# Optimization experiments

Measured on AMD Instinct MI355X. Metric: run time of the kernel, lower is better.

Reference implementation:

```python
import jax, jax.numpy as jnp
import numpy as np

B, T = 512, 200
N_SKILLS, M, DK, DV, H = 1000, 50, 64, 64, 128


def setup_inputs() -> dict:
    key = jax.random.key(0)
    ks = jax.random.split(key, 12)
    inp = {
        'skill_seq': jax.random.randint(ks[0], (B, T), 0, N_SKILLS, dtype=jnp.int32),
        'correct_seq': jax.random.randint(ks[1], (B, T), 0, 2, dtype=jnp.int32),
        'mask': jnp.ones((B, T), dtype=jnp.float32),
        'skill_embed': jax.random.normal(ks[2], (N_SKILLS, DK), dtype=jnp.float32),
        'key_memory': jax.random.normal(ks[3], (M, DK), dtype=jnp.float32) * 0.1,
        'value_init': jnp.zeros((M, DV), dtype=jnp.float32),
        'interaction_embed': jax.random.normal(ks[4], (2 * N_SKILLS, DV), dtype=jnp.float32),
        'erase_W': jax.random.normal(ks[5], (DV, DV), dtype=jnp.float32) * 0.05,
        'erase_b': jnp.zeros((DV,), dtype=jnp.float32),
        'add_W': jax.random.normal(ks[6], (DV, DV), dtype=jnp.float32) * 0.05,
        'add_b': jnp.zeros((DV,), dtype=jnp.float32),
        'fc1_W': jax.random.normal(ks[7], (DK + DV, H), dtype=jnp.float32) * 0.05,
        'fc1_b': jnp.zeros((H,), dtype=jnp.float32),
        'fc2_W': jax.random.normal(ks[8], (H, 1), dtype=jnp.float32) * 0.05,
        'fc2_b': jnp.zeros((1,), dtype=jnp.float32),
    }
    return inp


def reference(skill_seq, correct_seq, mask, skill_embed, key_memory, value_init,
              interaction_embed, erase_W, erase_b, add_W, add_b,
              fc1_W, fc1_b, fc2_W, fc2_b):
    n_skills = skill_embed.shape[0]
    b = skill_seq.shape[0]
    # Time-invariant-per-step quantities are precomputed vectorized over (B,T):
    q = skill_embed[skill_seq]                                   # (B,T,dk)
    w = jax.nn.softmax(jnp.einsum('btk,mk->btm', q, key_memory), axis=-1)  # (B,T,M)
    v = interaction_embed[skill_seq + correct_seq * n_skills]    # (B,T,dv)
    e = jax.nn.sigmoid(v @ erase_W + erase_b)                    # (B,T,dv)
    a = jnp.tanh(v @ add_W + add_b)                              # (B,T,dv)

    def step(mem, inputs):
        # mem: (B,M,dv); read BEFORE write, matching the torch loop
        w_t, e_t, a_t = inputs                                   # (B,M),(B,dv),(B,dv)
        read = jnp.einsum('bm,bmv->bv', w_t, mem)                # (B,dv)
        we = w_t[:, :, None]                                     # (B,M,1)
        mem = mem * (1.0 - we * e_t[:, None, :]) + we * a_t[:, None, :]
        return mem, read

    mem0 = jnp.broadcast_to(value_init, (b,) + value_init.shape)
    _, reads = jax.lax.scan(step, mem0,
                            (jnp.swapaxes(w, 0, 1), jnp.swapaxes(e, 0, 1), jnp.swapaxes(a, 0, 1)))
    reads = jnp.swapaxes(reads, 0, 1)                            # (B,T,dv)

    x = jnp.concatenate([q, reads], axis=-1)                     # (B,T,dk+dv)
    h = jax.nn.relu(x @ fc1_W + fc1_b)
    logit = (h @ fc2_W + fc2_b)[..., 0]
    p = jax.nn.sigmoid(logit)
    return p * mask, correct_seq.astype(jnp.float32) * mask
```

## Files before the change

### kernel.cpp

```cpp
#include <hip/hip_runtime.h>
#include <hip/hip_bf16.h>

#define B_  512
#define T_  200
#define NS  1000
#define M_  50
#define DK  64
#define DV  64
#define H_  128
#define NPOS (B_ * T_)

typedef __hip_bfloat16 bf16;
typedef unsigned short ushort_t;
typedef __bf16 bf16x8 __attribute__((ext_vector_type(8)));
typedef float  f32x4  __attribute__((ext_vector_type(4)));

__device__ __forceinline__ float ldf(const void* p, int i, int isbf) {
    return isbf ? __bfloat162float(((const bf16*)p)[i]) : ((const float*)p)[i];
}
__device__ __forceinline__ int sniff(const void* mask) {
    return (*(const unsigned*)mask == 0x3F800000u) ? 0 : 1;
}
__device__ __forceinline__ float rl(float x, int l) {
    return __int_as_float(__builtin_amdgcn_readlane(__float_as_int(x), l));
}
__device__ __forceinline__ ushort_t f2bf(float v) {
    bf16 h = __float2bfloat16(v);
    return *(ushort_t*)&h;
}

__global__ __launch_bounds__(256) void dk25_tabs(
    const void* __restrict__ mask,
    const void* __restrict__ skill_embed, const void* __restrict__ key_memory,
    const void* __restrict__ inter,
    const void* __restrict__ eW, const void* __restrict__ eb,
    const void* __restrict__ aW, const void* __restrict__ ab,
    const void* __restrict__ fc1W, const void* __restrict__ fc1b,
    float* __restrict__ w_tab, unsigned* __restrict__ ea_tab,
    float* __restrict__ hq_tab, ushort_t* __restrict__ W2f) {
    int isbf = sniff(mask);
    int lane = threadIdx.x & 63;
    int gwid = (blockIdx.x << 2) | (threadIdx.x >> 6);

    if (gwid < NS) {
        int s = gwid;
        float q = ldf(skill_embed, s * DK + lane, isbf);
        float acc = 0.f;
        if (lane < M_) {
            #pragma unroll 16
            for (int k = 0; k < DK; ++k)
                acc = fmaf(rl(q, k), ldf(key_memory, lane * DK + k, isbf), acc);
        }
        float val = (lane < M_) ? acc : -1e30f;
        float mx = val;
        #pragma unroll
        for (int off = 1; off < 64; off <<= 1) mx = fmaxf(mx, __shfl_xor(mx, off, 64));
        float ex = (lane < M_) ? __expf(val - mx) : 0.f;
        float sm = ex;
        #pragma unroll
        for (int off = 1; off < 64; off <<= 1) sm += __shfl_xor(sm, off, 64);
        w_tab[s * 64 + lane] = (lane < M_) ? ex / sm : 0.f;
    } else if (gwid < 3 * NS) {
        int r = gwid - NS;
        float vv = ldf(inter, r * DV + lane, isbf);
        float eacc = ldf(eb, lane, isbf);
        float aacc = ldf(ab, lane, isbf);
        #pragma unroll 16
        for (int u = 0; u < DV; ++u) {
            float vu = rl(vv, u);
            eacc = fmaf(vu, ldf(eW, u * DV + lane, isbf), eacc);
            aacc = fmaf(vu, ldf(aW, u * DV + lane, isbf), aacc);
        }
        float ev = 1.f / (1.f + __expf(-eacc));
        float av = tanhf(aacc);
        ea_tab[r * 64 + lane] = ((unsigned)f2bf(av) << 16) | (unsigned)f2bf(ev);
    } else if (gwid < 4 * NS) {
        int s = gwid - 3 * NS;
        float q = ldf(skill_embed, s * DK + lane, isbf);
        float acc0 = ldf(fc1b, lane, isbf);
        float acc1 = ldf(fc1b, 64 + lane, isbf);
        #pragma unroll 16
        for (int k = 0; k < DK; ++k) {
            float qk = rl(q, k);
            acc0 = fmaf(qk, ldf(fc1W, k * H_ + lane, isbf), acc0);
            acc1 = fmaf(qk, ldf(fc1W, k * H_ + 64 + lane, isbf), acc1);
        }
        hq_tab[s * H_ + lane]      = acc0;
        hq_tab[s * H_ + 64 + lane] = acc1;
    } else if (gwid < 4 * NS + 16) {
        int f = gwid - 4 * NS;
        int tile = f >> 1, kk = f & 1;
        int n = tile * 16 + (lane & 15);
        #pragma unroll
        for (int j = 0; j < 8; ++j) {
            int v = kk * 32 + (lane >> 4) * 8 + j;
            W2f[(f * 64 + lane) * 8 + j] = f2bf(ldf(fc1W, (DK + v) * H_ + n, isbf));
        }
    }
}


#define WAITV(N) \
    asm volatile("s_waitcnt vmcnt(" #N ")" ::: "memory"); \
    __builtin_amdgcn_sched_barrier(0);

#define GLL(gsrc, ldst) \
    __builtin_amdgcn_global_load_lds( \
        (const __attribute__((address_space(1))) void*)(const void*)(gsrc), \
        (__attribute__((address_space(3))) void*)(void*)(ldst), 4, 0, 0);

#define ISSUE(NB) { \
    _Pragma("unroll") \
    for (int st = 0; st < 8; ++st) { \
        const float*    wsrc_  = w_tab  + sI[st] * 64 + lane; \
        const unsigned* easrc_ = ea_tab + (sI[st] + cI[st] * NS) * 64 + lane; \
        GLL(wsrc_,  &ldsw[NB][st][0]) \
        GLL(easrc_, &ldsea[NB][st][0]) \
    } }

#define SCROW(W, MEM) \
    acc0 = fmaf(W.x, MEM.x, acc0); \
    acc1 = fmaf(W.y, MEM.y, acc1); \
    acc2 = fmaf(W.z, MEM.z, acc2); \
    acc3 = fmaf(W.w, MEM.w, acc3); \
    MEM.x = fmaf(-W.x, fmaf(e0, MEM.x, -a0), MEM.x); \
    MEM.y = fmaf(-W.y, fmaf(e0, MEM.y, -a0), MEM.y); \
    MEM.z = fmaf(-W.z, fmaf(e0, MEM.z, -a0), MEM.z); \
    MEM.w = fmaf(-W.w, fmaf(e0, MEM.w, -a0), MEM.w);

#define PSTEP(NB, TP) { \
    unsigned ea = ldsea[NB][TP][lane]; \
    float e0 = __uint_as_float(ea << 16); \
    float a0 = __uint_as_float(ea & 0xFFFF0000u); \
    float acc0 = 0.f, acc1 = 0.f, acc2 = 0.f, acc3 = 0.f; \
    { float4 w = ldsw[NB][TP][4 * k + 0]; SCROW(w, mem[0]) } \
    { float4 w = ldsw[NB][TP][4 * k + 1]; SCROW(w, mem[1]) } \
    { float4 w = ldsw[NB][TP][4 * k + 2]; SCROW(w, mem[2]) } \
    { float4 w = ldsw[NB][TP][4 * k + 3]; SCROW(w, mem[3]) } \
    read_bf[outbase + (TP) * 256] = f2bf((acc0 + acc1) + (acc2 + acc3)); }

__global__ __launch_bounds__(64, 2) void dk25_scan(
    const int*  __restrict__ ss, const int* __restrict__ cs,
    const void* __restrict__ mask, const void* __restrict__ value_init,
    const float* __restrict__ w_tab, const unsigned* __restrict__ ea_tab,
    ushort_t* __restrict__ read_bf) {

    __shared__ float4   ldsw[2][8][16];
    __shared__ unsigned ldsea[2][8][64];

    int isbf = sniff(mask);
    int lane = threadIdx.x;
    int bk   = blockIdx.x;
    int b    = bk >> 2, k = bk & 3;
    const int base = b * T_;

    float4 mem[4];
    #pragma unroll
    for (int i = 0; i < 4; ++i) {
        int r = 16 * k + 4 * i;
        mem[i].x = (r + 0 < M_) ? ldf(value_init, (r + 0) * DV + lane, isbf) : 0.f;
        mem[i].y = (r + 1 < M_) ? ldf(value_init, (r + 1) * DV + lane, isbf) : 0.f;
        mem[i].z = (r + 2 < M_) ? ldf(value_init, (r + 2) * DV + lane, isbf) : 0.f;
        mem[i].w = (r + 3 < M_) ? ldf(value_init, (r + 3) * DV + lane, isbf) : 0.f;
    }

    int sI[8], cI[8];

    #pragma unroll
    for (int st = 0; st < 8; ++st) { sI[st] = ss[base + st];     cI[st] = cs[base + st]; }
    ISSUE(0)
    #pragma unroll
    for (int st = 0; st < 8; ++st) { sI[st] = ss[base + 8 + st]; cI[st] = cs[base + 8 + st]; }
    ISSUE(1)

    size_t outbase = ((size_t)base * 4 + k) * 64 + lane;

    for (int cc = 0; cc < 25; ++cc) {
        int nb = cc & 1;
        int tb2 = 8 * (cc + 2); if (tb2 > T_ - 8) tb2 = T_ - 8;
        #pragma unroll
        for (int st = 0; st < 8; ++st) {
            sI[st] = ss[base + tb2 + st]; cI[st] = cs[base + tb2 + st];
        }
        WAITV(16)
        PSTEP(nb, 0) PSTEP(nb, 1) PSTEP(nb, 2) PSTEP(nb, 3)
        PSTEP(nb, 4) PSTEP(nb, 5) PSTEP(nb, 6) PSTEP(nb, 7)
        __builtin_amdgcn_sched_barrier(0);
        ISSUE(nb)
        __builtin_amdgcn_sched_barrier(0);
        outbase += 2048;
    }
}

#define FOR8(X) X(0) X(1) X(2) X(3) X(4) X(5) X(6) X(7)
#define DECL_C(t)  f32x4 c##t = {0.f, 0.f, 0.f, 0.f};
#define LOADB(t) bf16x8 b##t##_0 = B8[(2 * (t)) * 64 + lane], \
                        b##t##_1 = B8[(2 * (t) + 1) * 64 + lane];
#define FCKK(kk, p) { \
    bf16x8 av = A8[col * 32 + (kk) * 4 + quad]; \
    c0 = __builtin_amdgcn_mfma_f32_16x16x32_bf16(av, b0_##p, c0, 0, 0, 0); \
    c1 = __builtin_amdgcn_mfma_f32_16x16x32_bf16(av, b1_##p, c1, 0, 0, 0); \
    c2 = __builtin_amdgcn_mfma_f32_16x16x32_bf16(av, b2_##p, c2, 0, 0, 0); \
    c3 = __builtin_amdgcn_mfma_f32_16x16x32_bf16(av, b3_##p, c3, 0, 0, 0); \
    c4 = __builtin_amdgcn_mfma_f32_16x16x32_bf16(av, b4_##p, c4, 0, 0, 0); \
    c5 = __builtin_amdgcn_mfma_f32_16x16x32_bf16(av, b5_##p, c5, 0, 0, 0); \
    c6 = __builtin_amdgcn_mfma_f32_16x16x32_bf16(av, b6_##p, c6, 0, 0, 0); \
    c7 = __builtin_amdgcn_mfma_f32_16x16x32_bf16(av, b7_##p, c7, 0, 0, 0); }
#define EPI(t) { \
    float h; \
    h = c##t.x + hq_tab[s0r * H_ + t * 16 + col]; x0 = fmaf(fmaxf(h, 0.f), f2w##t, x0); \
    h = c##t.y + hq_tab[s1r * H_ + t * 16 + col]; x1 = fmaf(fmaxf(h, 0.f), f2w##t, x1); \
    h = c##t.z + hq_tab[s2r * H_ + t * 16 + col]; x2 = fmaf(fmaxf(h, 0.f), f2w##t, x2); \
    h = c##t.w + hq_tab[s3r * H_ + t * 16 + col]; x3 = fmaf(fmaxf(h, 0.f), f2w##t, x3); }

__global__ __launch_bounds__(64)
__attribute__((amdgpu_waves_per_eu(3))) void dk25_fc(
    const int*  __restrict__ skill_seq, const int* __restrict__ correct_seq,
    const void* __restrict__ mask,
    const void* __restrict__ fc2W, const void* __restrict__ fc2b,
    const float* __restrict__ hq_tab, const ushort_t* __restrict__ W2f,
    const ushort_t* __restrict__ read_bf,
    float* __restrict__ out0, float* __restrict__ out1) {

    int isbf = sniff(mask);
    int lane = threadIdx.x;
    int col  = lane & 15, quad = lane >> 4;

    const bf16x8* B8 = (const bf16x8*)W2f;
    FOR8(LOADB)

    float f2w0 = ldf(fc2W,   0 + col, isbf), f2w1 = ldf(fc2W,  16 + col, isbf);
    float f2w2 = ldf(fc2W,  32 + col, isbf), f2w3 = ldf(fc2W,  48 + col, isbf);
    float f2w4 = ldf(fc2W,  64 + col, isbf), f2w5 = ldf(fc2W,  80 + col, isbf);
    float f2w6 = ldf(fc2W,  96 + col, isbf), f2w7 = ldf(fc2W, 112 + col, isbf);
    float f2b  = ldf(fc2b, 0, isbf);

    for (int pg = blockIdx.x; pg < NPOS / 16; pg += gridDim.x) {
        int p0 = pg * 16;
        const bf16x8* A8 = (const bf16x8*)(read_bf + (size_t)p0 * 256);

        int s0r = skill_seq[p0 + quad * 4 + 0];
        int s1r = skill_seq[p0 + quad * 4 + 1];
        int s2r = skill_seq[p0 + quad * 4 + 2];
        int s3r = skill_seq[p0 + quad * 4 + 3];

        FOR8(DECL_C)
        FCKK(0, 0) FCKK(1, 1) FCKK(2, 0) FCKK(3, 1)
        FCKK(4, 0) FCKK(5, 1) FCKK(6, 0) FCKK(7, 1)

        float x0 = 0.f, x1 = 0.f, x2 = 0.f, x3 = 0.f;
        FOR8(EPI)

        #pragma unroll
        for (int off = 1; off < 16; off <<= 1) {
            x0 += __shfl_xor(x0, off, 64);
            x1 += __shfl_xor(x1, off, 64);
            x2 += __shfl_xor(x2, off, 64);
            x3 += __shfl_xor(x3, off, 64);
        }

        float mk0 = ldf(mask, p0 + quad * 4 + 0, isbf);
        float mk1 = ldf(mask, p0 + quad * 4 + 1, isbf);
        float mk2 = ldf(mask, p0 + quad * 4 + 2, isbf);
        float mk3 = ldf(mask, p0 + quad * 4 + 3, isbf);
        if (col == 0) {
            out0[p0 + quad * 4 + 0] = mk0 / (1.f + __expf(-(x0 + f2b)));
            out0[p0 + quad * 4 + 1] = mk1 / (1.f + __expf(-(x1 + f2b)));
            out0[p0 + quad * 4 + 2] = mk2 / (1.f + __expf(-(x2 + f2b)));
            out0[p0 + quad * 4 + 3] = mk3 / (1.f + __expf(-(x3 + f2b)));
        }
        if (col == 1) {
            out1[p0 + quad * 4 + 0] = (float)correct_seq[p0 + quad * 4 + 0] * mk0;
            out1[p0 + quad * 4 + 1] = (float)correct_seq[p0 + quad * 4 + 1] * mk1;
            out1[p0 + quad * 4 + 2] = (float)correct_seq[p0 + quad * 4 + 2] * mk2;
            out1[p0 + quad * 4 + 3] = (float)correct_seq[p0 + quad * 4 + 3] * mk3;
        }
    }
}

extern "C" void kernel_launch(void* const* d_in, const int* in_sizes, int n_in,
                              void* d_out, int out_size, void* d_ws, size_t ws_size,
                              hipStream_t stream) {
    const int*  skill_seq   = (const int*)d_in[0];
    const int*  correct_seq = (const int*)d_in[1];
    const void* mask        = d_in[2];
    const void* skill_embed = d_in[3];
    const void* key_memory  = d_in[4];
    const void* value_init  = d_in[5];
    const void* inter       = d_in[6];
    const void* erase_W     = d_in[7];
    const void* erase_b     = d_in[8];
    const void* add_W       = d_in[9];
    const void* add_b       = d_in[10];
    const void* fc1_W       = d_in[11];
    const void* fc1_b       = d_in[12];
    const void* fc2_W       = d_in[13];
    const void* fc2_b       = d_in[14];
    float* out = (float*)d_out;

    float*    ws      = (float*)d_ws + 16;
    float*    w_tab   = ws;
    unsigned* ea_tab  = (unsigned*)(ws + 64000);
    float*    hq_tab  = ws + 192000;
    ushort_t* W2f     = (ushort_t*)(ws + 320000);
    ushort_t* read_bf = (ushort_t*)(ws + 336400);

    dk25_tabs<<<1004, 256, 0, stream>>>(mask, skill_embed, key_memory, inter,
                                        erase_W, erase_b, add_W, add_b,
                                        fc1_W, fc1_b,
                                        w_tab, ea_tab, hq_tab, W2f);

    dk25_scan<<<B_ * 4, 64, 0, stream>>>(skill_seq, correct_seq, mask, value_init,
                                         w_tab, ea_tab, read_bf);

    dk25_fc<<<3200, 64, 0, stream>>>(skill_seq, correct_seq, mask,
                                     fc2_W, fc2_b, hq_tab, W2f, read_bf,
                                     out, out + (size_t)NPOS);
}
```

Before: 196.0 us.

## Replace LDS-staged scan prefetch with register double-buffered loads; permute hq table

The scan kernel no longer stages w and erase/add rows through LDS with global_load_lds and manual vmcnt waits. It keeps two register sets (A/B) and refills one directly from global memory right after each step consumes it, prefetching indices a chunk ahead. The hq table is also stored in a permuted layout so the FC epilogue fetches each row's hq values with two vector loads instead of eight scalar gathers. The scan change removes LDS traffic and waits but leaves only one step of latency hiding, so load stalls may surface.

```diff
diff --git a/kernel.cpp b/kernel.cpp
--- a/kernel.cpp
+++ b/kernel.cpp
@@ -29,7 +29,7 @@
     return *(ushort_t*)&h;
 }
 
-__global__ __launch_bounds__(256) void dk25_tabs(
+__global__ __launch_bounds__(256) void dk27_tabs(
     const void* __restrict__ mask,
     const void* __restrict__ skill_embed, const void* __restrict__ key_memory,
     const void* __restrict__ inter,
@@ -37,7 +37,7 @@
     const void* __restrict__ aW, const void* __restrict__ ab,
     const void* __restrict__ fc1W, const void* __restrict__ fc1b,
     float* __restrict__ w_tab, unsigned* __restrict__ ea_tab,
-    float* __restrict__ hq_tab, ushort_t* __restrict__ W2f) {
+    float* __restrict__ hq2, ushort_t* __restrict__ W2f) {
     int isbf = sniff(mask);
     int lane = threadIdx.x & 63;
     int gwid = (blockIdx.x << 2) | (threadIdx.x >> 6);
@@ -85,8 +85,8 @@
             acc0 = fmaf(qk, ldf(fc1W, k * H_ + lane, isbf), acc0);
             acc1 = fmaf(qk, ldf(fc1W, k * H_ + 64 + lane, isbf), acc1);
         }
-        hq_tab[s * H_ + lane]      = acc0;
-        hq_tab[s * H_ + 64 + lane] = acc1;
+        hq2[s * H_ + (lane & 15) * 8 +     (lane >> 4)] = acc0;
+        hq2[s * H_ + (lane & 15) * 8 + 4 + (lane >> 4)] = acc1;
     } else if (gwid < 4 * NS + 16) {
         int f = gwid - 4 * NS;
         int tile = f >> 1, kk = f & 1;
@@ -99,24 +99,6 @@
     }
 }
 
-
-#define WAITV(N) \
-    asm volatile("s_waitcnt vmcnt(" #N ")" ::: "memory"); \
-    __builtin_amdgcn_sched_barrier(0);
-
-#define GLL(gsrc, ldst) \
-    __builtin_amdgcn_global_load_lds( \
-        (const __attribute__((address_space(1))) void*)(const void*)(gsrc), \
-        (__attribute__((address_space(3))) void*)(void*)(ldst), 4, 0, 0);
-
-#define ISSUE(NB) { \
-    _Pragma("unroll") \
-    for (int st = 0; st < 8; ++st) { \
-        const float*    wsrc_  = w_tab  + sI[st] * 64 + lane; \
-        const unsigned* easrc_ = ea_tab + (sI[st] + cI[st] * NS) * 64 + lane; \
-        GLL(wsrc_,  &ldsw[NB][st][0]) \
-        GLL(easrc_, &ldsea[NB][st][0]) \
-    } }
 
 #define SCROW(W, MEM) \
     acc0 = fmaf(W.x, MEM.x, acc0); \
@@ -128,25 +110,29 @@
     MEM.z = fmaf(-W.z, fmaf(e0, MEM.z, -a0), MEM.z); \
     MEM.w = fmaf(-W.w, fmaf(e0, MEM.w, -a0), MEM.w);
 
-#define PSTEP(NB, TP) { \
-    unsigned ea = ldsea[NB][TP][lane]; \
-    float e0 = __uint_as_float(ea << 16); \
-    float a0 = __uint_as_float(ea & 0xFFFF0000u); \
+#define VPTR(P) { size_t u_ = (size_t)(P); asm volatile("" : "+v"(u_)); \
+                  (P) = (const f32x4*)u_; }
+
+#define REFILL(ST, S, C) { \
+    const f32x4* p_ = (const f32x4*)w_tab + (S) * 16 + 4 * k; \
+    VPTR(p_) \
+    w##ST##0 = p_[0]; w##ST##1 = p_[1]; w##ST##2 = p_[2]; w##ST##3 = p_[3]; \
+    ea##ST = ea_tab[((S) + (C) * NS) * 64 + lane]; }
+
+#define STEP(ST, TP) { \
+    float e0 = __uint_as_float(ea##ST << 16); \
+    float a0 = __uint_as_float(ea##ST & 0xFFFF0000u); \
     float acc0 = 0.f, acc1 = 0.f, acc2 = 0.f, acc3 = 0.f; \
-    { float4 w = ldsw[NB][TP][4 * k + 0]; SCROW(w, mem[0]) } \
-    { float4 w = ldsw[NB][TP][4 * k + 1]; SCROW(w, mem[1]) } \
-    { float4 w = ldsw[NB][TP][4 * k + 2]; SCROW(w, mem[2]) } \
-    { float4 w = ldsw[NB][TP][4 * k + 3]; SCROW(w, mem[3]) } \
-    read_bf[outbase + (TP) * 256] = f2bf((acc0 + acc1) + (acc2 + acc3)); }
-
-__global__ __launch_bounds__(64, 2) void dk25_scan(
+    SCROW(w##ST##0, mem[0]) SCROW(w##ST##1, mem[1]) \
+    SCROW(w##ST##2, mem[2]) SCROW(w##ST##3, mem[3]) \
+    read_bf[outb + (TP) * 256] = f2bf((acc0 + acc1) + (acc2 + acc3)); \
+    REFILL(ST, curS[TP], curC[TP]) }
+
+__global__ __launch_bounds__(64, 2) void dk27_scan(
     const int*  __restrict__ ss, const int* __restrict__ cs,
     const void* __restrict__ mask, const void* __restrict__ value_init,
     const float* __restrict__ w_tab, const unsigned* __restrict__ ea_tab,
     ushort_t* __restrict__ read_bf) {
-
-    __shared__ float4   ldsw[2][8][16];
-    __shared__ unsigned ldsea[2][8][64];
 
     int isbf = sniff(mask);
     int lane = threadIdx.x;
@@ -164,31 +150,33 @@
         mem[i].w = (r + 3 < M_) ? ldf(value_init, (r + 3) * DV + lane, isbf) : 0.f;
     }
 
-    int sI[8], cI[8];
-
+    int curS[8], curC[8], nxtS[8], nxtC[8];
     #pragma unroll
-    for (int st = 0; st < 8; ++st) { sI[st] = ss[base + st];     cI[st] = cs[base + st]; }
-    ISSUE(0)
-    #pragma unroll
-    for (int st = 0; st < 8; ++st) { sI[st] = ss[base + 8 + st]; cI[st] = cs[base + 8 + st]; }
-    ISSUE(1)
-
-    size_t outbase = ((size_t)base * 4 + k) * 64 + lane;
+    for (int j = 0; j < 8; ++j) { nxtS[j] = ss[base + 2 + j]; nxtC[j] = cs[base + 2 + j]; }
+
+    f32x4 wA0, wA1, wA2, wA3, wB0, wB1, wB2, wB3;
+    unsigned eaA, eaB;
+    {
+        int s_ = ss[base + 0], c_ = cs[base + 0];
+        REFILL(A, s_, c_)
+        s_ = ss[base + 1]; c_ = cs[base + 1];
+        REFILL(B, s_, c_)
+    }
+
+    size_t outb = ((size_t)base * 4 + k) * 64 + lane;
 
     for (int cc = 0; cc < 25; ++cc) {
-        int nb = cc & 1;
-        int tb2 = 8 * (cc + 2); if (tb2 > T_ - 8) tb2 = T_ - 8;
-        #pragma unroll
-        for (int st = 0; st < 8; ++st) {
-            sI[st] = ss[base + tb2 + st]; cI[st] = cs[base + tb2 + st];
-        }
-        WAITV(16)
-        PSTEP(nb, 0) PSTEP(nb, 1) PSTEP(nb, 2) PSTEP(nb, 3)
-        PSTEP(nb, 4) PSTEP(nb, 5) PSTEP(nb, 6) PSTEP(nb, 7)
-        __builtin_amdgcn_sched_barrier(0);
-        ISSUE(nb)
-        __builtin_amdgcn_sched_barrier(0);
-        outbase += 2048;
+        #pragma unroll
+        for (int j = 0; j < 8; ++j) { curS[j] = nxtS[j]; curC[j] = nxtC[j]; }
+        int tb = 8 * cc + 10;
+        #pragma unroll
+        for (int j = 0; j < 8; ++j) {
+            int tf = tb + j; tf = tf < T_ ? tf : T_ - 1;
+            nxtS[j] = ss[base + tf]; nxtC[j] = cs[base + tf];
+        }
+        STEP(A, 0) STEP(B, 1) STEP(A, 2) STEP(B, 3)
+        STEP(A, 4) STEP(B, 5) STEP(A, 6) STEP(B, 7)
+        outb += 2048;
     }
 }
 
@@ -206,19 +194,20 @@
     c5 = __builtin_amdgcn_mfma_f32_16x16x32_bf16(av, b5_##p, c5, 0, 0, 0); \
     c6 = __builtin_amdgcn_mfma_f32_16x16x32_bf16(av, b6_##p, c6, 0, 0, 0); \
     c7 = __builtin_amdgcn_mfma_f32_16x16x32_bf16(av, b7_##p, c7, 0, 0, 0); }
+#define HQ(r, t) (((t) < 4) ? qa##r[(t) & 3] : qb##r[(t) & 3])
 #define EPI(t) { \
     float h; \
-    h = c##t.x + hq_tab[s0r * H_ + t * 16 + col]; x0 = fmaf(fmaxf(h, 0.f), f2w##t, x0); \
-    h = c##t.y + hq_tab[s1r * H_ + t * 16 + col]; x1 = fmaf(fmaxf(h, 0.f), f2w##t, x1); \
-    h = c##t.z + hq_tab[s2r * H_ + t * 16 + col]; x2 = fmaf(fmaxf(h, 0.f), f2w##t, x2); \
-    h = c##t.w + hq_tab[s3r * H_ + t * 16 + col]; x3 = fmaf(fmaxf(h, 0.f), f2w##t, x3); }
+    h = c##t.x + HQ(0, t); x0 = fmaf(fmaxf(h, 0.f), f2w##t, x0); \
+    h = c##t.y + HQ(1, t); x1 = fmaf(fmaxf(h, 0.f), f2w##t, x1); \
+    h = c##t.z + HQ(2, t); x2 = fmaf(fmaxf(h, 0.f), f2w##t, x2); \
+    h = c##t.w + HQ(3, t); x3 = fmaf(fmaxf(h, 0.f), f2w##t, x3); }
 
 __global__ __launch_bounds__(64)
-__attribute__((amdgpu_waves_per_eu(3))) void dk25_fc(
+__attribute__((amdgpu_waves_per_eu(3))) void dk27_fc(
     const int*  __restrict__ skill_seq, const int* __restrict__ correct_seq,
     const void* __restrict__ mask,
     const void* __restrict__ fc2W, const void* __restrict__ fc2b,
-    const float* __restrict__ hq_tab, const ushort_t* __restrict__ W2f,
+    const float* __restrict__ hq2, const ushort_t* __restrict__ W2f,
     const ushort_t* __restrict__ read_bf,
     float* __restrict__ out0, float* __restrict__ out1) {
 
@@ -243,6 +232,15 @@
         int s1r = skill_seq[p0 + quad * 4 + 1];
         int s2r = skill_seq[p0 + quad * 4 + 2];
         int s3r = skill_seq[p0 + quad * 4 + 3];
+
+        f32x4 qa0 = *(const f32x4*)(hq2 + s0r * H_ + col * 8);
+        f32x4 qb0 = *(const f32x4*)(hq2 + s0r * H_ + col * 8 + 4);
+        f32x4 qa1 = *(const f32x4*)(hq2 + s1r * H_ + col * 8);
+        f32x4 qb1 = *(const f32x4*)(hq2 + s1r * H_ + col * 8 + 4);
+        f32x4 qa2 = *(const f32x4*)(hq2 + s2r * H_ + col * 8);
+        f32x4 qb2 = *(const f32x4*)(hq2 + s2r * H_ + col * 8 + 4);
+        f32x4 qa3 = *(const f32x4*)(hq2 + s3r * H_ + col * 8);
+        f32x4 qb3 = *(const f32x4*)(hq2 + s3r * H_ + col * 8 + 4);
 
         FOR8(DECL_C)
         FCKK(0, 0) FCKK(1, 1) FCKK(2, 0) FCKK(3, 1)
@@ -301,19 +299,19 @@
     float*    ws      = (float*)d_ws + 16;
     float*    w_tab   = ws;
     unsigned* ea_tab  = (unsigned*)(ws + 64000);
-    float*    hq_tab  = ws + 192000;
+    float*    hq2     = ws + 192000;
     ushort_t* W2f     = (ushort_t*)(ws + 320000);
     ushort_t* read_bf = (ushort_t*)(ws + 336400);
 
-    dk25_tabs<<<1004, 256, 0, stream>>>(mask, skill_embed, key_memory, inter,
+    dk27_tabs<<<1004, 256, 0, stream>>>(mask, skill_embed, key_memory, inter,
                                         erase_W, erase_b, add_W, add_b,
                                         fc1_W, fc1_b,
-                                        w_tab, ea_tab, hq_tab, W2f);
-
-    dk25_scan<<<B_ * 4, 64, 0, stream>>>(skill_seq, correct_seq, mask, value_init,
+                                        w_tab, ea_tab, hq2, W2f);
+
+    dk27_scan<<<B_ * 4, 64, 0, stream>>>(skill_seq, correct_seq, mask, value_init,
                                          w_tab, ea_tab, read_bf);
 
-    dk25_fc<<<3200, 64, 0, stream>>>(skill_seq, correct_seq, mask,
-                                     fc2_W, fc2_b, hq_tab, W2f, read_bf,
+    dk27_fc<<<3200, 64, 0, stream>>>(skill_seq, correct_seq, mask,
+                                     fc2_W, fc2_b, hq2, W2f, read_bf,
                                      out, out + (size_t)NPOS);
 }
```

Measured after the change: 197.8 us. About the same (+0.9%).
